# Kernel optimization log

Measured on AMD Instinct MI355X. Metric: run time of the kernel, lower is better.

## Reference

```python
import jax, jax.numpy as jnp
import numpy as np

S, N, H = 4096, 32, 512

def setup_inputs() -> dict:
    key = jax.random.key(0)
    ks = jax.random.split(key, 8)
    scale = 1.0 / np.sqrt(H)
    return {
        "hidden": jax.random.normal(ks[0], (N, H), dtype=jnp.float32),
        "encoder_outputs": jax.random.normal(ks[1], (S, N, H), dtype=jnp.float32),
        "W_w": jax.random.uniform(ks[2], (H, H), jnp.float32, -scale, scale),
        "W_b": jax.random.uniform(ks[3], (H,), jnp.float32, -scale, scale),
        "U_w": jax.random.uniform(ks[4], (H, H), jnp.float32, -scale, scale),
        "U_b": jax.random.uniform(ks[5], (H,), jnp.float32, -scale, scale),
        "v_w": jax.random.uniform(ks[6], (1, H), jnp.float32, -scale, scale),
        "v_b": jax.random.uniform(ks[7], (1,), jnp.float32, -scale, scale),
    }

def reference(hidden, encoder_outputs, W_w, W_b, U_w, U_b, v_w, v_b):
    # W(hidden): [N,H] -> broadcast over seq dim (equivalent to expand then Linear)
    wh = hidden @ W_w.T + W_b                      # [N, H]
    ue = jnp.einsum('snh,kh->snk', encoder_outputs, U_w) + U_b  # [S, N, H]
    energy = jnp.tanh(wh[None, :, :] + ue)         # [S, N, H]
    score = jnp.einsum('snh,oh->sno', energy, v_w) + v_b        # [S, N, 1]
    attention_weights = jax.nn.softmax(score, axis=0)           # softmax over seq
    context = jnp.sum(attention_weights * encoder_outputs, axis=0)  # [N, H]
    return (context, attention_weights)
```

## Files before the change

kernel.cpp:

```cpp
#include <hip/hip_runtime.h>

#define Sdim 4096
#define Ndim 32
#define Hdim 512
#define Mdim (Sdim * Ndim)

#define BM 64
#define BK 32
#define APAD 8

typedef __bf16 bf16x8 __attribute__((ext_vector_type(8)));
typedef float f32x4 __attribute__((ext_vector_type(4)));

__device__ __forceinline__ unsigned short f2bf(float f) {
    union { float f; unsigned u; } x;
    x.f = f;
    unsigned r = x.u + 0x7fffu + ((x.u >> 16) & 1u);
    return (unsigned short)(r >> 16);
}

__device__ __forceinline__ void load_lds16(const void* g, void* l) {
    __builtin_amdgcn_global_load_lds(
        (const __attribute__((address_space(1))) void*)g,
        (__attribute__((address_space(3))) void*)l, 16, 0, 0);
}

__device__ __forceinline__ float ftanh(float x) {
    float e = __expf(2.f * x);
    return 1.f - 2.f / (e + 1.f);
}

__global__ __launch_bounds__(256) void k_prep_bias(
    const float* __restrict__ hidden, const float* __restrict__ Ww,
    const float* __restrict__ Wb, const float* __restrict__ Ubias,
    float* __restrict__ bias) {
    const int idx = blockIdx.x * 256 + threadIdx.x;
    const int n = idx >> 9, c = idx & 511;
    const float4* hp = (const float4*)(hidden + n * Hdim);
    const float4* wp = (const float4*)(Ww + c * Hdim);
    float s = 0.f;
    for (int i = 0; i < Hdim / 4; ++i) {
        float4 a = hp[i], b = wp[i];
        s += a.x * b.x + a.y * b.y + a.z * b.z + a.w * b.w;
    }
    bias[idx] = s + Wb[c] + Ubias[c];
}

__global__ __launch_bounds__(256) void k_cvt(
    const float* __restrict__ src, unsigned short* __restrict__ dst) {
    const int i = blockIdx.x * 256 + threadIdx.x;
    float4 v = ((const float4*)src)[i];
    ushort4 u;
    u.x = f2bf(v.x); u.y = f2bf(v.y); u.z = f2bf(v.z); u.w = f2bf(v.w);
    ((ushort4*)dst)[i] = u;
}

__global__ __launch_bounds__(512, 4) void k_gemm_score(
    const float* __restrict__ enc,
    const unsigned short* __restrict__ Ub,
    const float* __restrict__ bias,
    const float* __restrict__ vw,
    const float* __restrict__ vbp,
    float* __restrict__ score) {
    __shared__ unsigned short Asm[BM][BK + APAD];
    __shared__ unsigned short Bsm[Hdim * BK];
    __shared__ float ssm[BM];

    const int t = threadIdx.x;
    const int lane = t & 63;
    const int w = t >> 6;
    const int c = lane & 15;
    const int q = lane >> 4;

    const int mBase = blockIdx.x * BM;

    if (t < BM) ssm[t] = 0.f;

    const int ar = t >> 3;
    const int ac = (t & 7) * 4;
    const float* aptr = enc + (size_t)(mBase + ar) * Hdim + ac;

    const int brow_in = lane >> 2;
    const int bchunk = (lane & 3) ^ (brow_in & 3);

    f32x4 acc[4][4];
#pragma unroll
    for (int i = 0; i < 4; ++i)
#pragma unroll
        for (int j = 0; j < 4; ++j) acc[i][j] = (f32x4){0.f, 0.f, 0.f, 0.f};

    for (int kk = 0; kk < Hdim / BK; ++kk) {
        const int k0 = kk * BK;
        __syncthreads();
        float4 av = *(const float4*)(aptr + k0);
        ushort4 u4;
        u4.x = f2bf(av.x); u4.y = f2bf(av.y); u4.z = f2bf(av.z); u4.w = f2bf(av.w);
        *(ushort4*)&Asm[ar][ac] = u4;
#pragma unroll
        for (int j = 0; j < 4; ++j) {
            const int row0 = w * 64 + j * 16;
            const unsigned short* g =
                Ub + (size_t)(row0 + brow_in) * Hdim + k0 + bchunk * 8;
            load_lds16(g, &Bsm[row0 * BK]);
        }
        __syncthreads();

        bf16x8 af[4], bfr[4];
#pragma unroll
        for (int mi = 0; mi < 4; ++mi)
            af[mi] = *(const bf16x8*)&Asm[mi * 16 + c][q * 8];
#pragma unroll
        for (int ni = 0; ni < 4; ++ni) {
            const int col = w * 64 + ni * 16 + c;
            const int chunk = q ^ (c & 3);
            bfr[ni] = *(const bf16x8*)&Bsm[col * BK + chunk * 8];
        }
#pragma unroll
        for (int mi = 0; mi < 4; ++mi)
#pragma unroll
            for (int ni = 0; ni < 4; ++ni)
                acc[mi][ni] = __builtin_amdgcn_mfma_f32_16x16x32_bf16(
                    af[mi], bfr[ni], acc[mi][ni], 0, 0, 0);
    }

    float vcol[4];
#pragma unroll
    for (int ni = 0; ni < 4; ++ni) vcol[ni] = vw[w * 64 + ni * 16 + c];

#pragma unroll
    for (int mi = 0; mi < 4; ++mi) {
#pragma unroll
        for (int reg = 0; reg < 4; ++reg) {
            const int r = mi * 16 + q * 4 + reg;
            const int n = r & 31;
            float p = 0.f;
#pragma unroll
            for (int ni = 0; ni < 4; ++ni) {
                const int col = w * 64 + ni * 16 + c;
                float e = acc[mi][ni][reg] + bias[n * Hdim + col];
                p += vcol[ni] * ftanh(e);
            }
            p += __shfl_xor(p, 1);
            p += __shfl_xor(p, 2);
            p += __shfl_xor(p, 4);
            p += __shfl_xor(p, 8);
            if (c == 0) atomicAdd(&ssm[r], p);
        }
    }
    __syncthreads();
    if (t < BM) {
        const int m = mBase + t;
        score[(m & 31) * Sdim + (m >> 5)] = ssm[t] + vbp[0];
    }
}

__global__ __launch_bounds__(256) void k_softmax(
    const float* __restrict__ score,
    float* __restrict__ wts,
    float* __restrict__ out_w) {
    const int n = blockIdx.x;
    const int t = threadIdx.x;
    const float* sc = score + n * Sdim;
    __shared__ float red[8];

    float mx = -1e30f;
    for (int i = t; i < Sdim; i += 256) mx = fmaxf(mx, sc[i]);
#pragma unroll
    for (int o = 32; o > 0; o >>= 1) mx = fmaxf(mx, __shfl_xor(mx, o));
    if ((t & 63) == 0) red[t >> 6] = mx;
    __syncthreads();
    mx = fmaxf(fmaxf(red[0], red[1]), fmaxf(red[2], red[3]));

    float sum = 0.f;
    for (int i = t; i < Sdim; i += 256) sum += __expf(sc[i] - mx);
#pragma unroll
    for (int o = 32; o > 0; o >>= 1) sum += __shfl_xor(sum, o);
    if ((t & 63) == 0) red[4 + (t >> 6)] = sum;
    __syncthreads();
    sum = red[4] + red[5] + red[6] + red[7];
    const float inv = 1.f / sum;
    for (int i = t; i < Sdim; i += 256) {
        float wv = __expf(sc[i] - mx) * inv;
        wts[n * Sdim + i] = wv;
        out_w[i * Ndim + n] = wv;
    }
}

__global__ __launch_bounds__(256) void k_context(
    const float* __restrict__ enc, const float* __restrict__ wts,
    float* __restrict__ ctx) {
    const int n = blockIdx.x & 31;
    const int s0 = (blockIdx.x >> 5) * 256;
    const int t = threadIdx.x;
    const int hv = t & 127;
    const int sl = t >> 7;
    float4 a = {0.f, 0.f, 0.f, 0.f};
    for (int i = sl; i < 256; i += 2) {
        const int s = s0 + i;
        const float wv = wts[n * Sdim + s];
        const float4 ev =
            *(const float4*)(enc + (size_t)(s * Ndim + n) * Hdim + hv * 4);
        a.x += wv * ev.x; a.y += wv * ev.y; a.z += wv * ev.z; a.w += wv * ev.w;
    }
    __shared__ float4 red[128];
    if (sl == 1) red[hv] = a;
    __syncthreads();
    if (sl == 0) {
        float4 o = red[hv];
        a.x += o.x; a.y += o.y; a.z += o.z; a.w += o.w;
        float* dst = ctx + n * Hdim + hv * 4;
        atomicAdd(dst + 0, a.x);
        atomicAdd(dst + 1, a.y);
        atomicAdd(dst + 2, a.z);
        atomicAdd(dst + 3, a.w);
    }
}

extern "C" void kernel_launch(void* const* d_in, const int* in_sizes, int n_in,
                              void* d_out, int out_size, void* d_ws,
                              size_t ws_size, hipStream_t stream) {
    const float* hidden = (const float*)d_in[0];
    const float* enc    = (const float*)d_in[1];
    const float* Ww     = (const float*)d_in[2];
    const float* Wb     = (const float*)d_in[3];
    const float* Uw     = (const float*)d_in[4];
    const float* Ubias  = (const float*)d_in[5];
    const float* vw     = (const float*)d_in[6];
    const float* vbp    = (const float*)d_in[7];

    float* out = (float*)d_out;

    char* ws = (char*)d_ws;
    float* bias          = (float*)(ws);
    unsigned short* Ub16 = (unsigned short*)(ws + 65536);
    float* score         = (float*)(ws + 65536 + 524288);
    float* wts           = (float*)(ws + 65536 + 2 * 524288);

    hipMemsetAsync(d_out, 0, Ndim * Hdim * sizeof(float), stream);
    k_prep_bias<<<64, 256, 0, stream>>>(hidden, Ww, Wb, Ubias, bias);
    k_cvt<<<256, 256, 0, stream>>>(Uw, Ub16);
    k_gemm_score<<<Mdim / BM, 512, 0, stream>>>(enc, Ub16, bias, vw, vbp, score);
    k_softmax<<<Ndim, 256, 0, stream>>>(score, wts, out + Ndim * Hdim);
    k_context<<<Ndim * (Sdim / 256), 256, 0, stream>>>(enc, wts, out);
}
```

Before: 576.4 us.

## Retile score GEMM into 128x256 blocks and replace context atomics with partial reduction

The score GEMM moves from 64-row tiles covering all 512 columns to 128x256 tiles split over two column halves, with a 2x4 wave grid, swizzled LDS and a per-column-half partial score buffer. Softmax sums the two partials, caches the row in LDS and writes only the output weights. Context then reads those weights directly, and its float atomics plus the memset are replaced by a partial-sum buffer and a separate reduce kernel. The bias prep kernel is restructured into a wave-per-column dot product, and the bf16 conversion now uses HIP intrinsics. The v_b bias is dropped from the score, which is valid because softmax is shift-invariant. The trade-off is that the encoder A tile is now read and converted twice, once per column half.

```diff
diff --git a/kernel.cpp b/kernel.cpp
--- a/kernel.cpp
+++ b/kernel.cpp
@@ -1,23 +1,18 @@
 #include <hip/hip_runtime.h>
+#include <hip/hip_bf16.h>
 
 #define Sdim 4096
 #define Ndim 32
 #define Hdim 512
 #define Mdim (Sdim * Ndim)
 
-#define BM 64
+#define BM 128
+#define BN 256
 #define BK 32
-#define APAD 8
 
 typedef __bf16 bf16x8 __attribute__((ext_vector_type(8)));
 typedef float f32x4 __attribute__((ext_vector_type(4)));
-
-__device__ __forceinline__ unsigned short f2bf(float f) {
-    union { float f; unsigned u; } x;
-    x.f = f;
-    unsigned r = x.u + 0x7fffu + ((x.u >> 16) & 1u);
-    return (unsigned short)(r >> 16);
-}
+typedef unsigned short ushort8v __attribute__((ext_vector_type(8)));
 
 __device__ __forceinline__ void load_lds16(const void* g, void* l) {
     __builtin_amdgcn_global_load_lds(
@@ -34,25 +29,31 @@
     const float* __restrict__ hidden, const float* __restrict__ Ww,
     const float* __restrict__ Wb, const float* __restrict__ Ubias,
     float* __restrict__ bias) {
-    const int idx = blockIdx.x * 256 + threadIdx.x;
-    const int n = idx >> 9, c = idx & 511;
-    const float4* hp = (const float4*)(hidden + n * Hdim);
-    const float4* wp = (const float4*)(Ww + c * Hdim);
-    float s = 0.f;
-    for (int i = 0; i < Hdim / 4; ++i) {
-        float4 a = hp[i], b = wp[i];
-        s += a.x * b.x + a.y * b.y + a.z * b.z + a.w * b.w;
-    }
-    bias[idx] = s + Wb[c] + Ubias[c];
+    const int t = threadIdx.x, w = t >> 6, lane = t & 63;
+    const int cc = blockIdx.x * 4 + w;
+    const float4 w0 = *(const float4*)(Ww + (size_t)cc * Hdim + lane * 8);
+    const float4 w1 = *(const float4*)(Ww + (size_t)cc * Hdim + lane * 8 + 4);
+    const float wb = Wb[cc] + Ubias[cc];
+    for (int n = 0; n < Ndim; ++n) {
+        const float4 h0 = *(const float4*)(hidden + n * Hdim + lane * 8);
+        const float4 h1 = *(const float4*)(hidden + n * Hdim + lane * 8 + 4);
+        float p = w0.x * h0.x + w0.y * h0.y + w0.z * h0.z + w0.w * h0.w +
+                  w1.x * h1.x + w1.y * h1.y + w1.z * h1.z + w1.w * h1.w;
+        p += __shfl_xor(p, 1);  p += __shfl_xor(p, 2);
+        p += __shfl_xor(p, 4);  p += __shfl_xor(p, 8);
+        p += __shfl_xor(p, 16); p += __shfl_xor(p, 32);
+        if (lane == 0) bias[n * Hdim + cc] = p + wb;
+    }
 }
 
 __global__ __launch_bounds__(256) void k_cvt(
     const float* __restrict__ src, unsigned short* __restrict__ dst) {
     const int i = blockIdx.x * 256 + threadIdx.x;
     float4 v = ((const float4*)src)[i];
-    ushort4 u;
-    u.x = f2bf(v.x); u.y = f2bf(v.y); u.z = f2bf(v.z); u.w = f2bf(v.w);
-    ((ushort4*)dst)[i] = u;
+    union { __hip_bfloat162 h[2]; ushort4 u; } r;
+    r.h[0] = __float22bfloat162_rn(make_float2(v.x, v.y));
+    r.h[1] = __float22bfloat162_rn(make_float2(v.z, v.w));
+    ((ushort4*)dst)[i] = r.u;
 }
 
 __global__ __launch_bounds__(512, 4) void k_gemm_score(
@@ -60,28 +61,40 @@
     const unsigned short* __restrict__ Ub,
     const float* __restrict__ bias,
     const float* __restrict__ vw,
-    const float* __restrict__ vbp,
-    float* __restrict__ score) {
-    __shared__ unsigned short Asm[BM][BK + APAD];
-    __shared__ unsigned short Bsm[Hdim * BK];
-    __shared__ float ssm[BM];
+    float* __restrict__ scorep) {
+    __shared__ __align__(16) unsigned short Asm[BM][40];
+    __shared__ __align__(16) unsigned short Bsm[BN * BK];
+    __shared__ float ssm[4][BM];
 
     const int t = threadIdx.x;
     const int lane = t & 63;
     const int w = t >> 6;
+    const int wM = w >> 2;
+    const int wN = w & 3;
     const int c = lane & 15;
     const int q = lane >> 4;
 
-    const int mBase = blockIdx.x * BM;
-
-    if (t < BM) ssm[t] = 0.f;
-
-    const int ar = t >> 3;
-    const int ac = (t & 7) * 4;
-    const float* aptr = enc + (size_t)(mBase + ar) * Hdim + ac;
-
-    const int brow_in = lane >> 2;
-    const int bchunk = (lane & 3) ^ (brow_in & 3);
+    const int rowblk = blockIdx.x >> 1;
+    const int colblk = blockIdx.x & 1;
+    const int mBase = rowblk * BM;
+    const int colBase = colblk * BN;
+
+    const int ar = t >> 2;
+    const int aq = t & 3;
+    const int asw = ((ar >> 3) & 1) << 1;
+    const float* aptr = enc + (size_t)(mBase + ar) * Hdim + aq * 8;
+    unsigned short* awr = &Asm[ar][(aq ^ asw) * 8];
+
+    const int bsw = (lane & 3) ^ ((lane >> 4) & 3);
+    const unsigned short* bptr0 =
+        Ub + (size_t)(colBase + w * 16 + (lane >> 2)) * Hdim + bsw * 8;
+    const unsigned short* bptr1 =
+        Ub + (size_t)(colBase + 128 + w * 16 + (lane >> 2)) * Hdim + bsw * 8;
+    unsigned short* bdst0 = &Bsm[(w * 16) * BK];
+    unsigned short* bdst1 = &Bsm[(128 + w * 16) * BK];
+
+    const int sA = ((c >> 3) & 1) << 1;
+    const int sB = c >> 2;
 
     f32x4 acc[4][4];
 #pragma unroll
@@ -90,30 +103,27 @@
         for (int j = 0; j < 4; ++j) acc[i][j] = (f32x4){0.f, 0.f, 0.f, 0.f};
 
     for (int kk = 0; kk < Hdim / BK; ++kk) {
-        const int k0 = kk * BK;
         __syncthreads();
-        float4 av = *(const float4*)(aptr + k0);
-        ushort4 u4;
-        u4.x = f2bf(av.x); u4.y = f2bf(av.y); u4.z = f2bf(av.z); u4.w = f2bf(av.w);
-        *(ushort4*)&Asm[ar][ac] = u4;
-#pragma unroll
-        for (int j = 0; j < 4; ++j) {
-            const int row0 = w * 64 + j * 16;
-            const unsigned short* g =
-                Ub + (size_t)(row0 + brow_in) * Hdim + k0 + bchunk * 8;
-            load_lds16(g, &Bsm[row0 * BK]);
-        }
+        const float4 f0 = *(const float4*)(aptr + kk * BK);
+        const float4 f1 = *(const float4*)(aptr + kk * BK + 4);
+        union { __hip_bfloat162 h[4]; ushort8v v; } pk;
+        pk.h[0] = __float22bfloat162_rn(make_float2(f0.x, f0.y));
+        pk.h[1] = __float22bfloat162_rn(make_float2(f0.z, f0.w));
+        pk.h[2] = __float22bfloat162_rn(make_float2(f1.x, f1.y));
+        pk.h[3] = __float22bfloat162_rn(make_float2(f1.z, f1.w));
+        *(ushort8v*)awr = pk.v;
+        load_lds16(bptr0 + kk * BK, bdst0);
+        load_lds16(bptr1 + kk * BK, bdst1);
         __syncthreads();
 
         bf16x8 af[4], bfr[4];
 #pragma unroll
         for (int mi = 0; mi < 4; ++mi)
-            af[mi] = *(const bf16x8*)&Asm[mi * 16 + c][q * 8];
+            af[mi] = *(const bf16x8*)&Asm[wM * 64 + mi * 16 + c][(q ^ sA) * 8];
 #pragma unroll
         for (int ni = 0; ni < 4; ++ni) {
-            const int col = w * 64 + ni * 16 + c;
-            const int chunk = q ^ (c & 3);
-            bfr[ni] = *(const bf16x8*)&Bsm[col * BK + chunk * 8];
+            const int col = wN * 64 + ni * 16 + c;
+            bfr[ni] = *(const bf16x8*)&Bsm[col * BK + (q ^ sB) * 8];
         }
 #pragma unroll
         for (int mi = 0; mi < 4; ++mi)
@@ -125,18 +135,18 @@
 
     float vcol[4];
 #pragma unroll
-    for (int ni = 0; ni < 4; ++ni) vcol[ni] = vw[w * 64 + ni * 16 + c];
+    for (int ni = 0; ni < 4; ++ni) vcol[ni] = vw[colBase + wN * 64 + ni * 16 + c];
 
 #pragma unroll
     for (int mi = 0; mi < 4; ++mi) {
 #pragma unroll
         for (int reg = 0; reg < 4; ++reg) {
-            const int r = mi * 16 + q * 4 + reg;
-            const int n = r & 31;
+            const int rl = wM * 64 + mi * 16 + q * 4 + reg;
+            const int n = rl & 31;
             float p = 0.f;
 #pragma unroll
             for (int ni = 0; ni < 4; ++ni) {
-                const int col = w * 64 + ni * 16 + c;
+                const int col = colBase + wN * 64 + ni * 16 + c;
                 float e = acc[mi][ni][reg] + bias[n * Hdim + col];
                 p += vcol[ni] * ftanh(e);
             }
@@ -144,76 +154,95 @@
             p += __shfl_xor(p, 2);
             p += __shfl_xor(p, 4);
             p += __shfl_xor(p, 8);
-            if (c == 0) atomicAdd(&ssm[r], p);
+            if (c == 0) ssm[wN][rl] = p;
         }
     }
     __syncthreads();
     if (t < BM) {
         const int m = mBase + t;
-        score[(m & 31) * Sdim + (m >> 5)] = ssm[t] + vbp[0];
+        const float s = ssm[0][t] + ssm[1][t] + ssm[2][t] + ssm[3][t];
+        scorep[colblk * Mdim + (m & 31) * Sdim + (m >> 5)] = s;
     }
 }
 
 __global__ __launch_bounds__(256) void k_softmax(
-    const float* __restrict__ score,
-    float* __restrict__ wts,
+    const float* __restrict__ scorep,
     float* __restrict__ out_w) {
     const int n = blockIdx.x;
     const int t = threadIdx.x;
-    const float* sc = score + n * Sdim;
+    const int w = t >> 6;
+    __shared__ float row[Sdim];
     __shared__ float red[8];
+    const float4* s0 = (const float4*)(scorep + n * Sdim);
+    const float4* s1 = (const float4*)(scorep + Mdim + n * Sdim);
 
     float mx = -1e30f;
-    for (int i = t; i < Sdim; i += 256) mx = fmaxf(mx, sc[i]);
+    for (int i = t; i < Sdim / 4; i += 256) {
+        float4 a = s0[i], b = s1[i];
+        float4 v;
+        v.x = a.x + b.x; v.y = a.y + b.y; v.z = a.z + b.z; v.w = a.w + b.w;
+        ((float4*)row)[i] = v;
+        mx = fmaxf(mx, fmaxf(fmaxf(v.x, v.y), fmaxf(v.z, v.w)));
+    }
 #pragma unroll
     for (int o = 32; o > 0; o >>= 1) mx = fmaxf(mx, __shfl_xor(mx, o));
-    if ((t & 63) == 0) red[t >> 6] = mx;
+    if ((t & 63) == 0) red[w] = mx;
     __syncthreads();
     mx = fmaxf(fmaxf(red[0], red[1]), fmaxf(red[2], red[3]));
 
     float sum = 0.f;
-    for (int i = t; i < Sdim; i += 256) sum += __expf(sc[i] - mx);
+    for (int i = t; i < Sdim; i += 256) sum += __expf(row[i] - mx);
 #pragma unroll
     for (int o = 32; o > 0; o >>= 1) sum += __shfl_xor(sum, o);
-    if ((t & 63) == 0) red[4 + (t >> 6)] = sum;
+    if ((t & 63) == 0) red[4 + w] = sum;
     __syncthreads();
     sum = red[4] + red[5] + red[6] + red[7];
     const float inv = 1.f / sum;
-    for (int i = t; i < Sdim; i += 256) {
-        float wv = __expf(sc[i] - mx) * inv;
-        wts[n * Sdim + i] = wv;
-        out_w[i * Ndim + n] = wv;
-    }
+    for (int i = t; i < Sdim; i += 256)
+        out_w[i * Ndim + n] = __expf(row[i] - mx) * inv;
 }
 
 __global__ __launch_bounds__(256) void k_context(
     const float* __restrict__ enc, const float* __restrict__ wts,
-    float* __restrict__ ctx) {
+    float* __restrict__ part) {
     const int n = blockIdx.x & 31;
-    const int s0 = (blockIdx.x >> 5) * 256;
+    const int sc = blockIdx.x >> 5;
+    const int s0 = sc * 256;
     const int t = threadIdx.x;
     const int hv = t & 127;
     const int sl = t >> 7;
-    float4 a = {0.f, 0.f, 0.f, 0.f};
-    for (int i = sl; i < 256; i += 2) {
-        const int s = s0 + i;
-        const float wv = wts[n * Sdim + s];
-        const float4 ev =
-            *(const float4*)(enc + (size_t)(s * Ndim + n) * Hdim + hv * 4);
-        a.x += wv * ev.x; a.y += wv * ev.y; a.z += wv * ev.z; a.w += wv * ev.w;
-    }
+    float4 a0 = {0.f, 0.f, 0.f, 0.f}, a1 = {0.f, 0.f, 0.f, 0.f};
+    for (int i = sl * 2; i < 256; i += 4) {
+        const float w0 = wts[(size_t)(s0 + i) * Ndim + n];
+        const float w1 = wts[(size_t)(s0 + i + 1) * Ndim + n];
+        const float4 e0 =
+            *(const float4*)(enc + ((size_t)(s0 + i) * Ndim + n) * Hdim + hv * 4);
+        const float4 e1 =
+            *(const float4*)(enc + ((size_t)(s0 + i + 1) * Ndim + n) * Hdim + hv * 4);
+        a0.x += w0 * e0.x; a0.y += w0 * e0.y; a0.z += w0 * e0.z; a0.w += w0 * e0.w;
+        a1.x += w1 * e1.x; a1.y += w1 * e1.y; a1.z += w1 * e1.z; a1.w += w1 * e1.w;
+    }
+    a0.x += a1.x; a0.y += a1.y; a0.z += a1.z; a0.w += a1.w;
     __shared__ float4 red[128];
-    if (sl == 1) red[hv] = a;
+    if (sl == 1) red[hv] = a0;
     __syncthreads();
     if (sl == 0) {
-        float4 o = red[hv];
-        a.x += o.x; a.y += o.y; a.z += o.z; a.w += o.w;
-        float* dst = ctx + n * Hdim + hv * 4;
-        atomicAdd(dst + 0, a.x);
-        atomicAdd(dst + 1, a.y);
-        atomicAdd(dst + 2, a.z);
-        atomicAdd(dst + 3, a.w);
-    }
+        const float4 b = red[hv];
+        float4 r;
+        r.x = a0.x + b.x; r.y = a0.y + b.y; r.z = a0.z + b.z; r.w = a0.w + b.w;
+        *(float4*)(part + (size_t)(sc * 32 + n) * Hdim + hv * 4) = r;
+    }
+}
+
+__global__ __launch_bounds__(256) void k_ctx_reduce(
+    const float* __restrict__ part, float* __restrict__ out) {
+    const int j = blockIdx.x * 256 + threadIdx.x;
+    float4 s = {0.f, 0.f, 0.f, 0.f};
+    for (int i = 0; i < 16; ++i) {
+        const float4 v = ((const float4*)part)[i * 4096 + j];
+        s.x += v.x; s.y += v.y; s.z += v.z; s.w += v.w;
+    }
+    ((float4*)out)[j] = s;
 }
 
 extern "C" void kernel_launch(void* const* d_in, const int* in_sizes, int n_in,
@@ -226,20 +255,21 @@
     const float* Uw     = (const float*)d_in[4];
     const float* Ubias  = (const float*)d_in[5];
     const float* vw     = (const float*)d_in[6];
-    const float* vbp    = (const float*)d_in[7];
 
     float* out = (float*)d_out;
 
     char* ws = (char*)d_ws;
     float* bias          = (float*)(ws);
-    unsigned short* Ub16 = (unsigned short*)(ws + 65536);
-    float* score         = (float*)(ws + 65536 + 524288);
-    float* wts           = (float*)(ws + 65536 + 2 * 524288);
-
-    hipMemsetAsync(d_out, 0, Ndim * Hdim * sizeof(float), stream);
-    k_prep_bias<<<64, 256, 0, stream>>>(hidden, Ww, Wb, Ubias, bias);
+    unsigned short* Ub16 = (unsigned short*)(ws + (64 << 10));
+    float* scorep        = (float*)(ws + (576 << 10));
+    float* part          = (float*)(ws + (64 << 10));
+
+    k_prep_bias<<<128, 256, 0, stream>>>(hidden, Ww, Wb, Ubias, bias);
     k_cvt<<<256, 256, 0, stream>>>(Uw, Ub16);
-    k_gemm_score<<<Mdim / BM, 512, 0, stream>>>(enc, Ub16, bias, vw, vbp, score);
-    k_softmax<<<Ndim, 256, 0, stream>>>(score, wts, out + Ndim * Hdim);
-    k_context<<<Ndim * (Sdim / 256), 256, 0, stream>>>(enc, wts, out);
-}
+    k_gemm_score<<<(Mdim / BM) * 2, 512, 0, stream>>>(enc, Ub16, bias, vw,
+                                                      scorep);
+    k_softmax<<<Ndim, 256, 0, stream>>>(scorep, out + Ndim * Hdim);
+    k_context<<<Ndim * (Sdim / 256), 256, 0, stream>>>(enc, out + Ndim * Hdim,
+                                                       part);
+    k_ctx_reduce<<<16, 256, 0, stream>>>(part, out);
+}
```

After: 537.1 us. -6.8%, faster.
